# Kernel tuning notes

Hardware: AMD Instinct MI355X
Metric: run time of the kernel (lower is better)

The kernel has to match this reference:

```python
import jax, jax.numpy as jnp
import numpy as np

BATCH = 8192
NUM_VECTORS = 512
LATENT_DIM = 64


def setup_inputs() -> dict:
    key = jax.random.key(0)
    k1, k2 = jax.random.split(key)
    x = jax.random.normal(k1, (BATCH, LATENT_DIM), dtype=jnp.float32)
    # glorot_uniform init for the codebook
    limit = np.sqrt(6.0 / (NUM_VECTORS + LATENT_DIM)).astype(np.float32)
    trainable_p = jax.random.uniform(
        k2, (NUM_VECTORS, LATENT_DIM), dtype=jnp.float32,
        minval=-limit, maxval=limit)
    return {"x": x, "trainable_p": trainable_p}


def reference(x, trainable_p):
    # distances: (batch, num_vectors) Euclidean cdist
    diff = x[:, None, :] - trainable_p[None, :, :]   # (B, V, D)
    distances = jnp.sqrt(jnp.sum(jnp.square(diff), axis=-1))
    # r1: min over batch for each codebook vector, then mean over codebook
    r1_cost = jnp.mean(jnp.min(distances, axis=0), axis=-1)
    # r2: min over codebook for each sample, then mean over batch
    r2_cost = jnp.mean(jnp.min(distances, axis=-1), axis=-1)
    return distances, r1_cost, r2_cost
```

## Files before the change

kernel.cpp:

```cpp
#include <hip/hip_runtime.h>

#define BATCH 8192
#define NV 512
#define LD 64

typedef __attribute__((ext_vector_type(8))) short bf16x8;
typedef __attribute__((ext_vector_type(4))) float f32x4;


static __device__ __forceinline__ short f2bf(float f) {
  unsigned u = __float_as_uint(f);
  u += 0x7fff + ((u >> 16) & 1);
  return (short)(u >> 16);
}

static __device__ __forceinline__ bf16x8 load8_bf16(const float* ptr) {
  float4 f0 = *(const float4*)(ptr);
  float4 f1 = *(const float4*)(ptr + 4);
  bf16x8 r;
  r[0] = f2bf(f0.x); r[1] = f2bf(f0.y); r[2] = f2bf(f0.z); r[3] = f2bf(f0.w);
  r[4] = f2bf(f1.x); r[5] = f2bf(f1.y); r[6] = f2bf(f1.z); r[7] = f2bf(f1.w);
  return r;
}

__global__ __launch_bounds__(256) void setup_kernel(const float* __restrict__ x,
                                                    const float* __restrict__ p,
                                                    unsigned* __restrict__ r1bits,
                                                    float* __restrict__ r2sum,
                                                    float* __restrict__ xnorm,
                                                    float* __restrict__ pnorm) {
  int tid = blockIdx.x * blockDim.x + threadIdx.x;
  if (tid < NV) r1bits[tid] = 0x7f800000u;
  if (tid == 0) *r2sum = 0.f;
  if (tid < BATCH) {
    const float4* xr = (const float4*)(x + tid * LD);
    float acc = 0.f;
#pragma unroll
    for (int i = 0; i < LD / 4; ++i) {
      float4 v = xr[i];
      acc = fmaf(v.x, v.x, acc); acc = fmaf(v.y, v.y, acc);
      acc = fmaf(v.z, v.z, acc); acc = fmaf(v.w, v.w, acc);
    }
    xnorm[tid] = acc;
  }
  if (tid < NV) {
    const float4* pr = (const float4*)(p + tid * LD);
    float acc = 0.f;
#pragma unroll
    for (int i = 0; i < LD / 4; ++i) {
      float4 v = pr[i];
      acc = fmaf(v.x, v.x, acc); acc = fmaf(v.y, v.y, acc);
      acc = fmaf(v.z, v.z, acc); acc = fmaf(v.w, v.w, acc);
    }
    pnorm[tid] = acc;
  }
}

__global__ __launch_bounds__(512) void dist_kernel(const float* __restrict__ x,
                                                   const float* __restrict__ p,
                                                   const float* __restrict__ xn,
                                                   const float* __restrict__ pn,
                                                   float* __restrict__ out,
                                                   unsigned* __restrict__ r1bits,
                                                   float* __restrict__ r2sum) {
  const int tid = threadIdx.x;
  const int w = tid >> 6;
  const int lane = tid & 63;
  const int lhi = lane >> 4;
  const int llo = lane & 15;
  const int r0 = blockIdx.x << 4;
  const int colbase = w * 64;

  __shared__ float r1buf[NV];
  __shared__ float r2buf[8][16];

  const float* arow = x + (r0 + llo) * LD;
  bf16x8 a0 = load8_bf16(arow + lhi * 8);
  bf16x8 a1 = load8_bf16(arow + 32 + lhi * 8);

  f32x4 acc0 = {0.f, 0.f, 0.f, 0.f}, acc1 = acc0, acc2 = acc0, acc3 = acc0;
  {
    const float* prow0 = p + (colbase + 0 * 16 + llo) * LD;
    acc0 = __builtin_amdgcn_mfma_f32_16x16x32_bf16(a0, load8_bf16(prow0 + lhi * 8), acc0, 0, 0, 0);
    acc0 = __builtin_amdgcn_mfma_f32_16x16x32_bf16(a1, load8_bf16(prow0 + 32 + lhi * 8), acc0, 0, 0, 0);
    const float* prow1 = p + (colbase + 1 * 16 + llo) * LD;
    acc1 = __builtin_amdgcn_mfma_f32_16x16x32_bf16(a0, load8_bf16(prow1 + lhi * 8), acc1, 0, 0, 0);
    acc1 = __builtin_amdgcn_mfma_f32_16x16x32_bf16(a1, load8_bf16(prow1 + 32 + lhi * 8), acc1, 0, 0, 0);
    const float* prow2 = p + (colbase + 2 * 16 + llo) * LD;
    acc2 = __builtin_amdgcn_mfma_f32_16x16x32_bf16(a0, load8_bf16(prow2 + lhi * 8), acc2, 0, 0, 0);
    acc2 = __builtin_amdgcn_mfma_f32_16x16x32_bf16(a1, load8_bf16(prow2 + 32 + lhi * 8), acc2, 0, 0, 0);
    const float* prow3 = p + (colbase + 3 * 16 + llo) * LD;
    acc3 = __builtin_amdgcn_mfma_f32_16x16x32_bf16(a0, load8_bf16(prow3 + lhi * 8), acc3, 0, 0, 0);
    acc3 = __builtin_amdgcn_mfma_f32_16x16x32_bf16(a1, load8_bf16(prow3 + 32 + lhi * 8), acc3, 0, 0, 0);
  }

  float xnr[4];
#pragma unroll
  for (int r = 0; r < 4; ++r) xnr[r] = xn[r0 + lhi * 4 + r];

  float rmin[4] = {3.4e38f, 3.4e38f, 3.4e38f, 3.4e38f};
  float cmin[4];
#pragma unroll
  for (int t = 0; t < 4; ++t) {
    const int col = colbase + t * 16 + llo;
    const float pnc = pn[col];
    const f32x4 a = (t == 0) ? acc0 : (t == 1) ? acc1 : (t == 2) ? acc2 : acc3;
    float cm = 3.4e38f;
#pragma unroll
    for (int r = 0; r < 4; ++r) {
      float d2 = xnr[r] + pnc - 2.f * a[r];
      float dist = sqrtf(fmaxf(d2, 0.f));
      out[(long)(r0 + lhi * 4 + r) * NV + col] = dist;
      cm = fminf(cm, dist);
      rmin[r] = fminf(rmin[r], dist);
    }
    cmin[t] = cm;
  }

#pragma unroll
  for (int t = 0; t < 4; ++t) {
    float v = cmin[t];
    v = fminf(v, __shfl_xor(v, 16));
    v = fminf(v, __shfl_xor(v, 32));
    if (lane < 16) r1buf[colbase + t * 16 + lane] = v;
  }
#pragma unroll
  for (int r = 0; r < 4; ++r) {
    float v = rmin[r];
    v = fminf(v, __shfl_xor(v, 1));
    v = fminf(v, __shfl_xor(v, 2));
    v = fminf(v, __shfl_xor(v, 4));
    v = fminf(v, __shfl_xor(v, 8));
    if (llo == 0) r2buf[w][lhi * 4 + r] = v;
  }
  __syncthreads();

  atomicMin(&r1bits[tid], __float_as_uint(r1buf[tid]));

  if (tid < 16) {
    float v = r2buf[0][tid];
#pragma unroll
    for (int ww = 1; ww < 8; ++ww) v = fminf(v, r2buf[ww][tid]);
    v += __shfl_xor(v, 1);
    v += __shfl_xor(v, 2);
    v += __shfl_xor(v, 4);
    v += __shfl_xor(v, 8);
    if (tid == 0) atomicAdd(r2sum, v);
  }
}

__global__ __launch_bounds__(512) void finalize_kernel(const unsigned* __restrict__ r1bits,
                                                       const float* __restrict__ r2sum,
                                                       float* __restrict__ out) {
  int tid = threadIdx.x;
  float val = __uint_as_float(r1bits[tid]);
#pragma unroll
  for (int o = 32; o; o >>= 1) val += __shfl_xor(val, o);
  __shared__ float ws[8];
  if ((tid & 63) == 0) ws[tid >> 6] = val;
  __syncthreads();
  if (tid == 0) {
    float s = 0.f;
    for (int w = 0; w < 8; ++w) s += ws[w];
    out[(long)BATCH * NV] = s / (float)NV;
    out[(long)BATCH * NV + 1] = r2sum[0] / (float)BATCH;
  }
}

extern "C" void kernel_launch(void* const* d_in, const int* in_sizes, int n_in,
                              void* d_out, int out_size, void* d_ws, size_t ws_size,
                              hipStream_t stream) {
  const float* x = (const float*)d_in[0];
  const float* p = (const float*)d_in[1];
  float* out = (float*)d_out;
  unsigned* r1bits = (unsigned*)d_ws;
  float* r2sum = (float*)d_ws + 512;
  float* xnorm = (float*)d_ws + 1024;
  float* pnorm = (float*)d_ws + 9216;

  hipLaunchKernelGGL(setup_kernel, dim3(BATCH / 256), dim3(256), 0, stream,
                     x, p, r1bits, r2sum, xnorm, pnorm);
  hipLaunchKernelGGL(dist_kernel, dim3(BATCH / 16), dim3(512), 0, stream,
                     x, p, xnorm, pnorm, out, r1bits, r2sum);
  hipLaunchKernelGGL(finalize_kernel, dim3(1), dim3(512), 0, stream,
                     r1bits, r2sum, out);
}
```

Measured before the change: 87.01 us.

## Fuse norm computation into distance kernel and issue r1 atomics per wave

```diff
diff --git a/kernel.cpp b/kernel.cpp
--- a/kernel.cpp
+++ b/kernel.cpp
@@ -14,116 +14,96 @@
   return (short)(u >> 16);
 }
 
-static __device__ __forceinline__ bf16x8 load8_bf16(const float* ptr) {
-  float4 f0 = *(const float4*)(ptr);
-  float4 f1 = *(const float4*)(ptr + 4);
+static __device__ __forceinline__ bf16x8 cvt8(float4 f0, float4 f1) {
   bf16x8 r;
   r[0] = f2bf(f0.x); r[1] = f2bf(f0.y); r[2] = f2bf(f0.z); r[3] = f2bf(f0.w);
   r[4] = f2bf(f1.x); r[5] = f2bf(f1.y); r[6] = f2bf(f1.z); r[7] = f2bf(f1.w);
   return r;
 }
 
-__global__ __launch_bounds__(256) void setup_kernel(const float* __restrict__ x,
-                                                    const float* __restrict__ p,
-                                                    unsigned* __restrict__ r1bits,
-                                                    float* __restrict__ r2sum,
-                                                    float* __restrict__ xnorm,
-                                                    float* __restrict__ pnorm) {
-  int tid = blockIdx.x * blockDim.x + threadIdx.x;
-  if (tid < NV) r1bits[tid] = 0x7f800000u;
-  if (tid == 0) *r2sum = 0.f;
-  if (tid < BATCH) {
-    const float4* xr = (const float4*)(x + tid * LD);
-    float acc = 0.f;
-#pragma unroll
-    for (int i = 0; i < LD / 4; ++i) {
-      float4 v = xr[i];
-      acc = fmaf(v.x, v.x, acc); acc = fmaf(v.y, v.y, acc);
-      acc = fmaf(v.z, v.z, acc); acc = fmaf(v.w, v.w, acc);
-    }
-    xnorm[tid] = acc;
-  }
-  if (tid < NV) {
-    const float4* pr = (const float4*)(p + tid * LD);
-    float acc = 0.f;
-#pragma unroll
-    for (int i = 0; i < LD / 4; ++i) {
-      float4 v = pr[i];
-      acc = fmaf(v.x, v.x, acc); acc = fmaf(v.y, v.y, acc);
-      acc = fmaf(v.z, v.z, acc); acc = fmaf(v.w, v.w, acc);
-    }
-    pnorm[tid] = acc;
-  }
+static __device__ __forceinline__ float sq16(float4 a, float4 b, float4 c, float4 d) {
+  float s = 0.f;
+  s = fmaf(a.x, a.x, s); s = fmaf(a.y, a.y, s); s = fmaf(a.z, a.z, s); s = fmaf(a.w, a.w, s);
+  s = fmaf(b.x, b.x, s); s = fmaf(b.y, b.y, s); s = fmaf(b.z, b.z, s); s = fmaf(b.w, b.w, s);
+  s = fmaf(c.x, c.x, s); s = fmaf(c.y, c.y, s); s = fmaf(c.z, c.z, s); s = fmaf(c.w, c.w, s);
+  s = fmaf(d.x, d.x, s); s = fmaf(d.y, d.y, s); s = fmaf(d.z, d.z, s); s = fmaf(d.w, d.w, s);
+  return s;
+}
+
+__global__ __launch_bounds__(512) void init_kernel(unsigned* __restrict__ r1bits,
+                                                   float* __restrict__ r2sum) {
+  r1bits[threadIdx.x] = 0x7f800000u;
+  if (threadIdx.x == 0) *r2sum = 0.f;
 }
 
 __global__ __launch_bounds__(512) void dist_kernel(const float* __restrict__ x,
                                                    const float* __restrict__ p,
-                                                   const float* __restrict__ xn,
-                                                   const float* __restrict__ pn,
                                                    float* __restrict__ out,
                                                    unsigned* __restrict__ r1bits,
                                                    float* __restrict__ r2sum) {
   const int tid = threadIdx.x;
-  const int w = tid >> 6;
-  const int lane = tid & 63;
-  const int lhi = lane >> 4;
-  const int llo = lane & 15;
+  const int w = tid >> 6, lane = tid & 63;
+  const int lhi = lane >> 4, llo = lane & 15;
   const int r0 = blockIdx.x << 4;
   const int colbase = w * 64;
 
-  __shared__ float r1buf[NV];
+  __shared__ float xn_s[8][16];
   __shared__ float r2buf[8][16];
 
   const float* arow = x + (r0 + llo) * LD;
-  bf16x8 a0 = load8_bf16(arow + lhi * 8);
-  bf16x8 a1 = load8_bf16(arow + 32 + lhi * 8);
+  float4 xa0 = *(const float4*)(arow + lhi * 8);
+  float4 xa1 = *(const float4*)(arow + lhi * 8 + 4);
+  float4 xa2 = *(const float4*)(arow + 32 + lhi * 8);
+  float4 xa3 = *(const float4*)(arow + 32 + lhi * 8 + 4);
 
-  f32x4 acc0 = {0.f, 0.f, 0.f, 0.f}, acc1 = acc0, acc2 = acc0, acc3 = acc0;
-  {
-    const float* prow0 = p + (colbase + 0 * 16 + llo) * LD;
-    acc0 = __builtin_amdgcn_mfma_f32_16x16x32_bf16(a0, load8_bf16(prow0 + lhi * 8), acc0, 0, 0, 0);
-    acc0 = __builtin_amdgcn_mfma_f32_16x16x32_bf16(a1, load8_bf16(prow0 + 32 + lhi * 8), acc0, 0, 0, 0);
-    const float* prow1 = p + (colbase + 1 * 16 + llo) * LD;
-    acc1 = __builtin_amdgcn_mfma_f32_16x16x32_bf16(a0, load8_bf16(prow1 + lhi * 8), acc1, 0, 0, 0);
-    acc1 = __builtin_amdgcn_mfma_f32_16x16x32_bf16(a1, load8_bf16(prow1 + 32 + lhi * 8), acc1, 0, 0, 0);
-    const float* prow2 = p + (colbase + 2 * 16 + llo) * LD;
-    acc2 = __builtin_amdgcn_mfma_f32_16x16x32_bf16(a0, load8_bf16(prow2 + lhi * 8), acc2, 0, 0, 0);
-    acc2 = __builtin_amdgcn_mfma_f32_16x16x32_bf16(a1, load8_bf16(prow2 + 32 + lhi * 8), acc2, 0, 0, 0);
-    const float* prow3 = p + (colbase + 3 * 16 + llo) * LD;
-    acc3 = __builtin_amdgcn_mfma_f32_16x16x32_bf16(a0, load8_bf16(prow3 + lhi * 8), acc3, 0, 0, 0);
-    acc3 = __builtin_amdgcn_mfma_f32_16x16x32_bf16(a1, load8_bf16(prow3 + 32 + lhi * 8), acc3, 0, 0, 0);
+  float s = sq16(xa0, xa1, xa2, xa3);
+  s += __shfl_xor(s, 16);
+  s += __shfl_xor(s, 32);
+  if (lhi == 0) xn_s[w][llo] = s;
+
+  bf16x8 a0 = cvt8(xa0, xa1), a1 = cvt8(xa2, xa3);
+
+  f32x4 acc[4];
+  float pns[4];
+#pragma unroll
+  for (int t = 0; t < 4; ++t) {
+    const float* prow = p + (colbase + t * 16 + llo) * LD;
+    float4 pf0 = *(const float4*)(prow + lhi * 8);
+    float4 pf1 = *(const float4*)(prow + lhi * 8 + 4);
+    float4 pf2 = *(const float4*)(prow + 32 + lhi * 8);
+    float4 pf3 = *(const float4*)(prow + 32 + lhi * 8 + 4);
+    float ps = sq16(pf0, pf1, pf2, pf3);
+    ps += __shfl_xor(ps, 16);
+    ps += __shfl_xor(ps, 32);
+    pns[t] = ps;
+    f32x4 z = {0.f, 0.f, 0.f, 0.f};
+    z = __builtin_amdgcn_mfma_f32_16x16x32_bf16(a0, cvt8(pf0, pf1), z, 0, 0, 0);
+    z = __builtin_amdgcn_mfma_f32_16x16x32_bf16(a1, cvt8(pf2, pf3), z, 0, 0, 0);
+    acc[t] = z;
   }
 
   float xnr[4];
 #pragma unroll
-  for (int r = 0; r < 4; ++r) xnr[r] = xn[r0 + lhi * 4 + r];
+  for (int r = 0; r < 4; ++r) xnr[r] = xn_s[w][lhi * 4 + r];
 
   float rmin[4] = {3.4e38f, 3.4e38f, 3.4e38f, 3.4e38f};
-  float cmin[4];
 #pragma unroll
   for (int t = 0; t < 4; ++t) {
     const int col = colbase + t * 16 + llo;
-    const float pnc = pn[col];
-    const f32x4 a = (t == 0) ? acc0 : (t == 1) ? acc1 : (t == 2) ? acc2 : acc3;
     float cm = 3.4e38f;
 #pragma unroll
     for (int r = 0; r < 4; ++r) {
-      float d2 = xnr[r] + pnc - 2.f * a[r];
+      float d2 = xnr[r] + pns[t] - 2.f * acc[t][r];
       float dist = sqrtf(fmaxf(d2, 0.f));
       out[(long)(r0 + lhi * 4 + r) * NV + col] = dist;
       cm = fminf(cm, dist);
       rmin[r] = fminf(rmin[r], dist);
     }
-    cmin[t] = cm;
+    cm = fminf(cm, __shfl_xor(cm, 16));
+    cm = fminf(cm, __shfl_xor(cm, 32));
+    if (lane < 16) atomicMin(&r1bits[colbase + t * 16 + lane], __float_as_uint(cm));
   }
 
-#pragma unroll
-  for (int t = 0; t < 4; ++t) {
-    float v = cmin[t];
-    v = fminf(v, __shfl_xor(v, 16));
-    v = fminf(v, __shfl_xor(v, 32));
-    if (lane < 16) r1buf[colbase + t * 16 + lane] = v;
-  }
 #pragma unroll
   for (int r = 0; r < 4; ++r) {
     float v = rmin[r];
@@ -134,9 +114,6 @@
     if (llo == 0) r2buf[w][lhi * 4 + r] = v;
   }
   __syncthreads();
-
-  atomicMin(&r1bits[tid], __float_as_uint(r1buf[tid]));
-
   if (tid < 16) {
     float v = r2buf[0][tid];
 #pragma unroll
@@ -160,9 +137,9 @@
   if ((tid & 63) == 0) ws[tid >> 6] = val;
   __syncthreads();
   if (tid == 0) {
-    float s = 0.f;
-    for (int w = 0; w < 8; ++w) s += ws[w];
-    out[(long)BATCH * NV] = s / (float)NV;
+    float sum = 0.f;
+    for (int w = 0; w < 8; ++w) sum += ws[w];
+    out[(long)BATCH * NV] = sum / (float)NV;
     out[(long)BATCH * NV + 1] = r2sum[0] / (float)BATCH;
   }
 }
@@ -175,13 +152,10 @@
   float* out = (float*)d_out;
   unsigned* r1bits = (unsigned*)d_ws;
   float* r2sum = (float*)d_ws + 512;
-  float* xnorm = (float*)d_ws + 1024;
-  float* pnorm = (float*)d_ws + 9216;
 
-  hipLaunchKernelGGL(setup_kernel, dim3(BATCH / 256), dim3(256), 0, stream,
-                     x, p, r1bits, r2sum, xnorm, pnorm);
+  hipLaunchKernelGGL(init_kernel, dim3(1), dim3(512), 0, stream, r1bits, r2sum);
   hipLaunchKernelGGL(dist_kernel, dim3(BATCH / 16), dim3(512), 0, stream,
-                     x, p, xnorm, pnorm, out, r1bits, r2sum);
+                     x, p, out, r1bits, r2sum);
   hipLaunchKernelGGL(finalize_kernel, dim3(1), dim3(512), 0, stream,
                      r1bits, r2sum, out);
 }
```

Measured after the change: 84.52 us. -2.9%, faster.
